# Kernel optimization log

Hardware: AMD Instinct MI355X
Metric: run time of the kernel (lower is better)

## Reference

```python
import jax, jax.numpy as jnp
import numpy as np

D = 768
HID = 4 * D
B = 16
HRES = 32
WRES = 32
T = HRES * WRES


def layernorm(x, g, b, eps=1e-5):
    m = jnp.mean(x, axis=-1, keepdims=True)
    v = jnp.mean(jnp.square(x - m), axis=-1, keepdims=True)
    return (x - m) * jax.lax.rsqrt(v + eps) * g + b


def q_shift(x, H, W):
    # Vision-RWKV quad-directional token shift: split channels into 4 groups,
    # each group takes the neighboring patch's value in one direction (zero pad).
    Bn, N, C = x.shape
    xi = x.reshape(Bn, H, W, C)
    c = C // 4
    g0 = jnp.pad(xi[:, :, :-1, 0 * c:1 * c], ((0, 0), (0, 0), (1, 0), (0, 0)))  # from left
    g1 = jnp.pad(xi[:, :, 1:, 1 * c:2 * c], ((0, 0), (0, 0), (0, 1), (0, 0)))   # from right
    g2 = jnp.pad(xi[:, :-1, :, 2 * c:3 * c], ((0, 0), (1, 0), (0, 0), (0, 0)))  # from above
    g3 = jnp.pad(xi[:, 1:, :, 3 * c:4 * c], ((0, 0), (0, 1), (0, 0), (0, 0)))   # from below
    return jnp.concatenate([g0, g1, g2, g3], axis=-1).reshape(Bn, N, C)


def wkv_scan(w_log, u, k, v):
    # Numerically stable RWKV WKV recurrence (per-channel linear attention).
    # k, v: [B, T, C]; w = -exp(w_log) is the per-channel decay, u the bonus.
    w = -jnp.exp(w_log)
    kT = jnp.swapaxes(k, 0, 1)  # [T, B, C]
    vT = jnp.swapaxes(v, 0, 1)
    Bn, C = k.shape[0], k.shape[2]
    aa0 = jnp.zeros((Bn, C), k.dtype)
    bb0 = jnp.zeros((Bn, C), k.dtype)
    pp0 = jnp.full((Bn, C), -1e30, k.dtype)

    def step(carry, kv):
        aa, bb, pp = carry
        kt, vt = kv
        ww = u + kt
        p = jnp.maximum(pp, ww)
        e1 = jnp.exp(pp - p)
        e2 = jnp.exp(ww - p)
        out = (e1 * aa + e2 * vt) / (e1 * bb + e2)
        ww2 = pp + w
        p2 = jnp.maximum(ww2, kt)
        e1b = jnp.exp(ww2 - p2)
        e2b = jnp.exp(kt - p2)
        return (e1b * aa + e2b * vt, e1b * bb + e2b, p2), out

    _, outT = jax.lax.scan(step, (aa0, bb0, pp0), (kT, vT))
    return jnp.swapaxes(outT, 0, 1)  # [B, T, C]


def setup_inputs() -> dict:
    key = jax.random.key(0)
    ks = jax.random.split(key, 16)

    def nrm(k, shape, s=0.02):
        return jax.random.normal(k, shape, jnp.float32) * s

    return {
        "x": jax.random.normal(ks[0], (B, T, D), jnp.float32),
        "H": HRES,
        "W": WRES,
        "ln1_g": jnp.ones((D,), jnp.float32),
        "ln1_b": jnp.zeros((D,), jnp.float32),
        "ln2_g": jnp.ones((D,), jnp.float32),
        "ln2_b": jnp.zeros((D,), jnp.float32),
        "mu_k": jax.random.uniform(ks[1], (D,), jnp.float32),
        "mu_v": jax.random.uniform(ks[2], (D,), jnp.float32),
        "mu_r": jax.random.uniform(ks[3], (D,), jnp.float32),
        "w_log": nrm(ks[4], (D,), 0.5),
        "u": nrm(ks[5], (D,), 0.5),
        "Wk": nrm(ks[6], (D, D)),
        "Wv": nrm(ks[7], (D, D)),
        "Wr": nrm(ks[8], (D, D)),
        "Wo": nrm(ks[9], (D, D)),
        "cmu_k": jax.random.uniform(ks[10], (D,), jnp.float32),
        "cmu_r": jax.random.uniform(ks[11], (D,), jnp.float32),
        "Ck": nrm(ks[12], (HID, D)),
        "Cv": nrm(ks[13], (D, HID)),
        "Cr": nrm(ks[14], (D, D)),
    }


def reference(x, H, W, ln1_g, ln1_b, ln2_g, ln2_b, mu_k, mu_v, mu_r, w_log, u,
              Wk, Wv, Wr, Wo, cmu_k, cmu_r, Ck, Cv, Cr):
    h = x
    # ---- spatial mix (RWKV time-mix over patch sequence) ----
    a = layernorm(h, ln1_g, ln1_b)
    sx = q_shift(a, H, W)
    xk = a * mu_k + sx * (1.0 - mu_k)
    xv = a * mu_v + sx * (1.0 - mu_v)
    xr = a * mu_r + sx * (1.0 - mu_r)
    k = xk @ Wk.T
    v = xv @ Wv.T
    r = jax.nn.sigmoid(xr @ Wr.T)
    wkv = wkv_scan(w_log, u, k, v)
    h = h + (r * wkv) @ Wo.T
    # ---- channel mix (squared-ReLU gated FFN) ----
    a2 = layernorm(h, ln2_g, ln2_b)
    sx2 = q_shift(a2, H, W)
    xk2 = a2 * cmu_k + sx2 * (1.0 - cmu_k)
    xr2 = a2 * cmu_r + sx2 * (1.0 - cmu_r)
    kk = jnp.square(jax.nn.relu(xk2 @ Ck.T))
    h = h + jax.nn.sigmoid(xr2 @ Cr.T) * (kk @ Cv.T)
    # ---- outer residual from RWKVBlock.forward ----
    return h + x
```

## Files before the change

### kernel.cpp

```cpp
#include <hip/hip_runtime.h>
#include <hip/hip_bf16.h>

#define DD   768
#define TT   1024
#define BBATCH 16
#define NROWS (BBATCH * TT)
#define HIDN 3072
#define HHALF 1536
#define HH 32
#define WW 32
#define DW  (DD * DD)
#define DH  (DD * HIDN)
#define CCH 64
#define PCH (TT / CCH)

typedef float  floatx4 __attribute__((ext_vector_type(4)));
typedef __bf16 bf16x8  __attribute__((ext_vector_type(8)));

__device__ __forceinline__ float bf2f(__hip_bfloat16 v) { return __bfloat162float(v); }
__device__ __forceinline__ __hip_bfloat16 f2bf(float v) { return __float2bfloat16(v); }
__device__ __forceinline__ float toF(__hip_bfloat16 v) { return __bfloat162float(v); }
__device__ __forceinline__ float toF(float v) { return v; }

__device__ __forceinline__ void load4f(const float* __restrict__ p, float o[4]) {
    const float4 v = *reinterpret_cast<const float4*>(p);
    o[0] = v.x; o[1] = v.y; o[2] = v.z; o[3] = v.w;
}
__device__ __forceinline__ void load4f(const __hip_bfloat16* __restrict__ p, float o[4]) {
    const ushort4 v = *reinterpret_cast<const ushort4*>(p);
    o[0] = bf2f(__hip_bfloat16_raw{v.x});
    o[1] = bf2f(__hip_bfloat16_raw{v.y});
    o[2] = bf2f(__hip_bfloat16_raw{v.z});
    o[3] = bf2f(__hip_bfloat16_raw{v.w});
}

#define GL2LDS(gp, lp)  __builtin_amdgcn_global_load_lds(                     \
    (const __attribute__((address_space(1))) void*)(gp),                      \
    (__attribute__((address_space(3))) void*)(lp), 16, 0, 0)

__global__ __launch_bounds__(256)
void cvt_all(const float* __restrict__ w0, const float* __restrict__ w1,
             const float* __restrict__ w2, const float* __restrict__ w3,
             const float* __restrict__ w4, const float* __restrict__ w5,
             const float* __restrict__ w6, __hip_bfloat16* __restrict__ dst)
{
    const int b = blockIdx.x;
    const float* s; size_t dofs; int rel;
    if (b < 2880) {
        const int seg = b / 576; rel = b - seg * 576;
        s = seg == 0 ? w0 : seg == 1 ? w1 : seg == 2 ? w2 : seg == 3 ? w3 : w4;
        dofs = (size_t)seg * DW;
    } else if (b < 5184) {
        rel = b - 2880; s = w5; dofs = 5ull * DW;
    } else {
        rel = b - 5184; s = w6; dofs = 5ull * DW + DH;
    }
    const int i = rel * 1024 + threadIdx.x * 4;
    const float4 v = *reinterpret_cast<const float4*>(s + i);
    __hip_bfloat16 o[4] = {f2bf(v.x), f2bf(v.y), f2bf(v.z), f2bf(v.w)};
    *reinterpret_cast<ushort4*>(&dst[dofs + i]) = *reinterpret_cast<const ushort4*>(o);
}

template <typename TIN>
__global__ __launch_bounds__(256)
void ln_stats_k(const TIN* __restrict__ x,
                float* __restrict__ mean, float* __restrict__ rstd)
{
    const int row  = blockIdx.x * 4 + (threadIdx.x >> 6);
    const int lane = threadIdx.x & 63;
    const TIN* xr = x + (size_t)row * DD;
    float s1 = 0.f, s2 = 0.f;
#pragma unroll
    for (int q = 0; q < 3; ++q) {
        float v4[4];
        load4f(xr + 4 * lane + 256 * q, v4);
#pragma unroll
        for (int e = 0; e < 4; ++e) { s1 += v4[e]; s2 += v4[e] * v4[e]; }
    }
#pragma unroll
    for (int off = 32; off > 0; off >>= 1) {
        s1 += __shfl_down(s1, off);
        s2 += __shfl_down(s2, off);
    }
    if (lane == 0) {
        const float m = s1 * (1.f / DD);
        mean[row] = m;
        rstd[row] = rsqrtf(s2 * (1.f / DD) - m * m + 1e-5f);
    }
}

template <typename TIN, int NOUT>
__global__ __launch_bounds__(256)
void mix_k(const TIN* __restrict__ x,
           const float* __restrict__ mean, const float* __restrict__ rstd,
           const float* __restrict__ g, const float* __restrict__ b,
           const float* __restrict__ muk,
           const float* __restrict__ muv,
           const float* __restrict__ mur,
           __hip_bfloat16* __restrict__ xk,
           __hip_bfloat16* __restrict__ xv,
           __hip_bfloat16* __restrict__ xr)
{
    const size_t i4 = ((size_t)blockIdx.x * 256 + threadIdx.x) * 4;
    const int c  = (int)(i4 % DD);
    const int n  = (int)((i4 / DD) % TT);
    const int bb = (int)(i4 / ((size_t)DD * TT));
    const int y = n >> 5, xp = n & 31;
    const int grow = bb * TT + n;

    const int grp = c / (DD / 4);
    int ny = y, nx = xp; bool ok;
    if      (grp == 0) { nx = xp - 1; ok = xp > 0;      }
    else if (grp == 1) { nx = xp + 1; ok = xp < WW - 1; }
    else if (grp == 2) { ny = y - 1;  ok = y > 0;       }
    else               { ny = y + 1;  ok = y < HH - 1;  }

    const float4 gv = *reinterpret_cast<const float4*>(g + c);
    const float4 bv = *reinterpret_cast<const float4*>(b + c);
    const float gg[4] = {gv.x, gv.y, gv.z, gv.w};
    const float bbv[4] = {bv.x, bv.y, bv.z, bv.w};

    float xc[4];
    load4f(x + (size_t)grow * DD + c, xc);
    const float m = mean[grow], rs = rstd[grow];
    float av[4], sx[4] = {0.f, 0.f, 0.f, 0.f};
#pragma unroll
    for (int e = 0; e < 4; ++e) av[e] = (xc[e] - m) * rs * gg[e] + bbv[e];

    if (ok) {
        const int nrow = bb * TT + ny * WW + nx;
        float xn[4];
        load4f(x + (size_t)nrow * DD + c, xn);
        const float m2 = mean[nrow], rs2 = rstd[nrow];
#pragma unroll
        for (int e = 0; e < 4; ++e) sx[e] = (xn[e] - m2) * rs2 * gg[e] + bbv[e];
    }

    const float4 mkv = *reinterpret_cast<const float4*>(muk + c);
    const float4 mrv = *reinterpret_cast<const float4*>(mur + c);
    const float mk[4] = {mkv.x, mkv.y, mkv.z, mkv.w};
    const float mr[4] = {mrv.x, mrv.y, mrv.z, mrv.w};
    __hip_bfloat16 ok4[4], or4[4];
#pragma unroll
    for (int e = 0; e < 4; ++e) {
        ok4[e] = f2bf(av[e] * mk[e] + sx[e] * (1.f - mk[e]));
        or4[e] = f2bf(av[e] * mr[e] + sx[e] * (1.f - mr[e]));
    }
    *reinterpret_cast<ushort4*>(&xk[i4]) = *reinterpret_cast<const ushort4*>(ok4);
    *reinterpret_cast<ushort4*>(&xr[i4]) = *reinterpret_cast<const ushort4*>(or4);
    if (NOUT == 3) {
        const float4 mvv = *reinterpret_cast<const float4*>(muv + c);
        const float mv[4] = {mvv.x, mvv.y, mvv.z, mvv.w};
        __hip_bfloat16 ov4[4];
#pragma unroll
        for (int e = 0; e < 4; ++e)
            ov4[e] = f2bf(av[e] * mv[e] + sx[e] * (1.f - mv[e]));
        *reinterpret_cast<ushort4*>(&xv[i4]) = *reinterpret_cast<const ushort4*>(ov4);
    }
}

#define BM 128
#define BN 128
#define BKK 64

__device__ __forceinline__ void gemm_core(
    const __hip_bfloat16* __restrict__ A, const __hip_bfloat16* __restrict__ W,
    int K, int Wstr, int bm, int bn, unsigned short* lds, floatx4 acc[4][4])
{
    const int tid  = threadIdx.x;
    const int lane = tid & 63, wid = tid >> 6;
    const int l15  = lane & 15, quad = lane >> 4;
    const int m0   = (wid & 1) * 64;
    const int n0   = (wid >> 1) * 64;
    const int srow  = lane >> 3;
    const int gcolg = (lane & 7) ^ srow;
    const int s0    = wid * 4;
    const int swzbase = l15 & 7;

    for (int k0 = 0; k0 < K; k0 += BKK) {
#pragma unroll
        for (int t = 0; t < 4; ++t) {
            const int s   = s0 + t;
            const int row = s * 8 + srow;
            GL2LDS(A + (size_t)(bm * BM + row) * K    + k0 + gcolg * 8,
                   &lds[s * 512]);
            GL2LDS(W + (size_t)(bn * BN + row) * Wstr + k0 + gcolg * 8,
                   &lds[8192 + s * 512]);
        }
        __syncthreads();
#pragma unroll
        for (int kk = 0; kk < BKK; kk += 32) {
            const int swz = (((kk >> 3) + quad) ^ swzbase) * 8;
            bf16x8 af[4], bfr[4];
#pragma unroll
            for (int i = 0; i < 4; ++i)
                af[i] = *reinterpret_cast<const bf16x8*>(
                    &lds[(m0 + i * 16 + l15) * BKK + swz]);
#pragma unroll
            for (int j = 0; j < 4; ++j)
                bfr[j] = *reinterpret_cast<const bf16x8*>(
                    &lds[8192 + (n0 + j * 16 + l15) * BKK + swz]);
#pragma unroll
            for (int i = 0; i < 4; ++i)
#pragma unroll
                for (int j = 0; j < 4; ++j)
                    acc[i][j] = __builtin_amdgcn_mfma_f32_16x16x32_bf16(
                        af[i], bfr[j], acc[i][j], 0, 0, 0);
        }
        __syncthreads();
    }
}

__device__ __forceinline__ void xpose_band(const floatx4 accRow[4], float* scr,
                                           int lane, float cv[16])
{
    const int l15 = lane & 15, quad = lane >> 4;
#pragma unroll
    for (int j = 0; j < 4; ++j)
#pragma unroll
        for (int r = 0; r < 4; ++r)
            scr[(quad * 4 + r) * 68 + j * 16 + l15] = accRow[j][r];
    const int row_l = lane >> 2, cb = (lane & 3) * 16;
#pragma unroll
    for (int q = 0; q < 4; ++q)
        *reinterpret_cast<float4*>(&cv[q * 4]) =
            *reinterpret_cast<const float4*>(&scr[row_l * 68 + cb + q * 4]);
}

template <int MODE>
__global__ __launch_bounds__(256, 2)
void gemm_bt(const __hip_bfloat16* __restrict__ A,
             const __hip_bfloat16* __restrict__ W,
             int K, int Wstr, int Nn,
             __hip_bfloat16* __restrict__ outB,
             float* __restrict__ outF,
             const __hip_bfloat16* __restrict__ auxS,
             const __hip_bfloat16* __restrict__ auxH,
             const float* __restrict__ auxX,
             const float* __restrict__ auxG)
{
    __shared__ __align__(16) unsigned short lds[16384];
    const int bm = blockIdx.x, bn = blockIdx.y;
    const int tid = threadIdx.x, lane = tid & 63, wid = tid >> 6;
    const int m0 = (wid & 1) * 64, n0 = (wid >> 1) * 64;

    floatx4 acc[4][4];
#pragma unroll
    for (int i = 0; i < 4; ++i)
#pragma unroll
        for (int j = 0; j < 4; ++j)
            acc[i][j] = floatx4{0.f, 0.f, 0.f, 0.f};

    gemm_core(A, W, K, Wstr, bm, bn, lds, acc);

    float* scr = reinterpret_cast<float*>(lds) + wid * 1088;
    const int row_l = lane >> 2, cb = (lane & 3) * 16;
#pragma unroll
    for (int i = 0; i < 4; ++i) {
        float cv[16];
        xpose_band(acc[i], scr, lane, cv);
        const int grow = bm * BM + m0 + i * 16 + row_l;
        const int gcol = bn * BN + n0 + cb;
        const size_t idx = (size_t)grow * Nn + gcol;
        if (MODE == 1 || MODE == 3) {
            __hip_bfloat16 ob[16];
#pragma unroll
            for (int e = 0; e < 16; ++e) {
                float v = cv[e];
                if (MODE == 1) v = 1.f / (1.f + __expf(-v));
                else { v = fmaxf(v, 0.f); v = v * v; }
                ob[e] = f2bf(v);
            }
            *reinterpret_cast<uint4*>(&outB[idx])     = *reinterpret_cast<const uint4*>(&ob[0]);
            *reinterpret_cast<uint4*>(&outB[idx + 8]) = *reinterpret_cast<const uint4*>(&ob[8]);
        } else if (MODE == 2) {
            float xv[16];
#pragma unroll
            for (int q = 0; q < 4; ++q)
                *reinterpret_cast<float4*>(&xv[q * 4]) =
                    *reinterpret_cast<const float4*>(&auxX[idx + q * 4]);
            __hip_bfloat16 ob[16];
#pragma unroll
            for (int e = 0; e < 16; ++e) ob[e] = f2bf(cv[e] + xv[e]);
            *reinterpret_cast<uint4*>(&outB[idx])     = *reinterpret_cast<const uint4*>(&ob[0]);
            *reinterpret_cast<uint4*>(&outB[idx + 8]) = *reinterpret_cast<const uint4*>(&ob[8]);
        } else if (MODE == 4) {
            unsigned short hs[16], ss[16]; float xv[16], ov[16];
            *reinterpret_cast<uint4*>(&hs[0]) = *reinterpret_cast<const uint4*>(&auxH[idx]);
            *reinterpret_cast<uint4*>(&hs[8]) = *reinterpret_cast<const uint4*>(&auxH[idx + 8]);
            *reinterpret_cast<uint4*>(&ss[0]) = *reinterpret_cast<const uint4*>(&auxS[idx]);
            *reinterpret_cast<uint4*>(&ss[8]) = *reinterpret_cast<const uint4*>(&auxS[idx + 8]);
#pragma unroll
            for (int q = 0; q < 4; ++q)
                *reinterpret_cast<float4*>(&xv[q * 4]) =
                    *reinterpret_cast<const float4*>(&auxX[idx + q * 4]);
#pragma unroll
            for (int e = 0; e < 16; ++e)
                ov[e] = bf2f(__hip_bfloat16_raw{hs[e]})
                      + bf2f(__hip_bfloat16_raw{ss[e]}) * cv[e] + xv[e];
#pragma unroll
            for (int q = 0; q < 4; ++q)
                *reinterpret_cast<float4*>(&outF[idx + q * 4]) =
                    *reinterpret_cast<const float4*>(&ov[q * 4]);
        } else if (MODE == 5) {
            unsigned short ss[16]; float ov[16];
            *reinterpret_cast<uint4*>(&ss[0]) = *reinterpret_cast<const uint4*>(&auxS[idx]);
            *reinterpret_cast<uint4*>(&ss[8]) = *reinterpret_cast<const uint4*>(&auxS[idx + 8]);
#pragma unroll
            for (int q = 0; q < 4; ++q)
                *reinterpret_cast<float4*>(&ov[q * 4]) =
                    *reinterpret_cast<const float4*>(&outF[idx + q * 4]);
#pragma unroll
            for (int e = 0; e < 16; ++e)
                ov[e] += bf2f(__hip_bfloat16_raw{ss[e]}) * cv[e];
#pragma unroll
            for (int q = 0; q < 4; ++q)
                *reinterpret_cast<float4*>(&outF[idx + q * 4]) =
                    *reinterpret_cast<const float4*>(&ov[q * 4]);
        } else if (MODE == 6) {
            unsigned short hs[16]; float xv[16], gf[16], ov[16];
            *reinterpret_cast<uint4*>(&hs[0]) = *reinterpret_cast<const uint4*>(&auxH[idx]);
            *reinterpret_cast<uint4*>(&hs[8]) = *reinterpret_cast<const uint4*>(&auxH[idx + 8]);
#pragma unroll
            for (int q = 0; q < 4; ++q) {
                *reinterpret_cast<float4*>(&xv[q * 4]) =
                    *reinterpret_cast<const float4*>(&auxX[idx + q * 4]);
                *reinterpret_cast<float4*>(&gf[q * 4]) =
                    *reinterpret_cast<const float4*>(&auxG[idx + q * 4]);
            }
#pragma unroll
            for (int e = 0; e < 16; ++e)
                ov[e] = bf2f(__hip_bfloat16_raw{hs[e]}) + gf[e] * cv[e] + xv[e];
#pragma unroll
            for (int q = 0; q < 4; ++q)
                *reinterpret_cast<float4*>(&outF[idx + q * 4]) =
                    *reinterpret_cast<const float4*>(&ov[q * 4]);
        } else {
            float ov[16];
#pragma unroll
            for (int e = 0; e < 16; ++e)
                ov[e] = 1.f / (1.f + __expf(-cv[e]));
#pragma unroll
            for (int q = 0; q < 4; ++q)
                *reinterpret_cast<float4*>(&outF[idx + q * 4]) =
                    *reinterpret_cast<const float4*>(&ov[q * 4]);
        }
    }
}

__global__ __launch_bounds__(256, 2)
void gemm_qkv(const __hip_bfloat16* __restrict__ A0, const __hip_bfloat16* __restrict__ A1,
              const __hip_bfloat16* __restrict__ A2,
              const __hip_bfloat16* __restrict__ W0, const __hip_bfloat16* __restrict__ W1,
              const __hip_bfloat16* __restrict__ W2,
              __hip_bfloat16* __restrict__ O0, __hip_bfloat16* __restrict__ O1,
              __hip_bfloat16* __restrict__ O2)
{
    __shared__ __align__(16) unsigned short lds[16384];
    const int z = blockIdx.z;
    const __hip_bfloat16* A = z == 0 ? A0 : z == 1 ? A1 : A2;
    const __hip_bfloat16* W = z == 0 ? W0 : z == 1 ? W1 : W2;
    __hip_bfloat16*       O = z == 0 ? O0 : z == 1 ? O1 : O2;
    const int bm = blockIdx.x, bn = blockIdx.y;
    const int tid = threadIdx.x, lane = tid & 63, wid = tid >> 6;
    const int m0 = (wid & 1) * 64, n0 = (wid >> 1) * 64;

    floatx4 acc[4][4];
#pragma unroll
    for (int i = 0; i < 4; ++i)
#pragma unroll
        for (int j = 0; j < 4; ++j)
            acc[i][j] = floatx4{0.f, 0.f, 0.f, 0.f};

    gemm_core(A, W, DD, DD, bm, bn, lds, acc);

    float* scr = reinterpret_cast<float*>(lds) + wid * 1088;
    const int row_l = lane >> 2, cb = (lane & 3) * 16;
#pragma unroll
    for (int i = 0; i < 4; ++i) {
        float cv[16];
        xpose_band(acc[i], scr, lane, cv);
        const int grow = bm * BM + m0 + i * 16 + row_l;
        const int gcol = bn * BN + n0 + cb;
        const size_t idx = (size_t)grow * DD + gcol;
        __hip_bfloat16 ob[16];
#pragma unroll
        for (int e = 0; e < 16; ++e) {
            float v = cv[e];
            if (z == 2) v = 1.f / (1.f + __expf(-v));
            ob[e] = f2bf(v);
        }
        *reinterpret_cast<uint4*>(&O[idx])     = *reinterpret_cast<const uint4*>(&ob[0]);
        *reinterpret_cast<uint4*>(&O[idx + 8]) = *reinterpret_cast<const uint4*>(&ob[8]);
    }
}

__global__ __launch_bounds__(256)
void wkv_passA(const float* __restrict__ w_log,
               const __hip_bfloat16* __restrict__ k,
               const __hip_bfloat16* __restrict__ v,
               float* __restrict__ SA, float* __restrict__ SB,
               float* __restrict__ SP)
{
    const int c  = blockIdx.x * 256 + threadIdx.x;
    const int j  = blockIdx.y;
    const int bb = blockIdx.z;
    const float w = -__expf(w_log[c]);
    const size_t base = ((size_t)bb * TT + j * CCH) * DD + c;
    float a = 0.f, b = 0.f, p = -1e30f;
#pragma unroll 4
    for (int t = 0; t < CCH; ++t) {
        const size_t o = base + (size_t)t * DD;
        const float kt = bf2f(k[o]);
        const float vt = bf2f(v[o]);
        const float ww2 = p + w;
        const float p2  = fmaxf(ww2, kt);
        const float e1  = __expf(ww2 - p2);
        const float e2  = __expf(kt - p2);
        a = e1 * a + e2 * vt;
        b = e1 * b + e2;
        p = p2;
    }
    const size_t si = ((size_t)bb * PCH + j) * DD + c;
    SA[si] = a; SB[si] = b; SP[si] = p;
}

__global__ __launch_bounds__(256)
void wkv_scanj(const float* __restrict__ w_log,
               float* __restrict__ SA, float* __restrict__ SB,
               float* __restrict__ SP)
{
    const int idx = blockIdx.x * 256 + threadIdx.x;
    const int c = idx % DD, bb = idx / DD;
    const float wC = -__expf(w_log[c]) * (float)CCH;
    float a = 0.f, b = 0.f, p = -1e30f;
#pragma unroll
    for (int j = 0; j < PCH; ++j) {
        const size_t si = ((size_t)bb * PCH + j) * DD + c;
        const float aj = SA[si], bj = SB[si], pj = SP[si];
        SA[si] = a; SB[si] = b; SP[si] = p;
        const float pd = p + wC;
        const float pn = fmaxf(pd, pj);
        const float e1 = __expf(pd - pn);
        const float e2 = __expf(pj - pn);
        a = e1 * a + e2 * aj;
        b = e1 * b + e2 * bj;
        p = pn;
    }
}

__global__ __launch_bounds__(256)
void wkv_passB(const float* __restrict__ w_log, const float* __restrict__ u,
               const __hip_bfloat16* __restrict__ k,
               const __hip_bfloat16* __restrict__ v,
               const __hip_bfloat16* __restrict__ r,
               __hip_bfloat16* __restrict__ rw,
               const float* __restrict__ SA, const float* __restrict__ SB,
               const float* __restrict__ SP)
{
    const int c  = blockIdx.x * 256 + threadIdx.x;
    const int j  = blockIdx.y;
    const int bb = blockIdx.z;
    const float w  = -__expf(w_log[c]);
    const float uu = u[c];
    const size_t si = ((size_t)bb * PCH + j) * DD + c;
    float aa = SA[si], bbv = SB[si], pp = SP[si];
    const size_t base = ((size_t)bb * TT + j * CCH) * DD + c;
#pragma unroll 4
    for (int t = 0; t < CCH; ++t) {
        const size_t o = base + (size_t)t * DD;
        const float kt = bf2f(k[o]);
        const float vt = bf2f(v[o]);
        const float rt = bf2f(r[o]);
        const float ww = uu + kt;
        const float p  = fmaxf(pp, ww);
        const float e1 = __expf(pp - p);
        const float e2 = __expf(ww - p);
        const float ov = __fdividef(e1 * aa + e2 * vt, e1 * bbv + e2);
        rw[o] = f2bf(rt * ov);
        const float ww2 = pp + w;
        const float p2  = fmaxf(ww2, kt);
        const float e1b = __expf(ww2 - p2);
        const float e2b = __expf(kt - p2);
        aa  = e1b * aa + e2b * vt;
        bbv = e1b * bbv + e2b;
        pp  = p2;
    }
}

extern "C" void kernel_launch(void* const* d_in, const int* in_sizes, int n_in,
                              void* d_out, int out_size, void* d_ws, size_t ws_size,
                              hipStream_t stream)
{
    (void)in_sizes; (void)n_in; (void)out_size;
    const float* x     = (const float*)d_in[0];
    const float* ln1_g = (const float*)d_in[3];
    const float* ln1_b = (const float*)d_in[4];
    const float* ln2_g = (const float*)d_in[5];
    const float* ln2_b = (const float*)d_in[6];
    const float* mu_k  = (const float*)d_in[7];
    const float* mu_v  = (const float*)d_in[8];
    const float* mu_r  = (const float*)d_in[9];
    const float* w_log = (const float*)d_in[10];
    const float* u     = (const float*)d_in[11];
    const float* Wk    = (const float*)d_in[12];
    const float* Wv    = (const float*)d_in[13];
    const float* Wr    = (const float*)d_in[14];
    const float* Wo    = (const float*)d_in[15];
    const float* cmu_k = (const float*)d_in[16];
    const float* cmu_r = (const float*)d_in[17];
    const float* Ck    = (const float*)d_in[18];
    const float* Cv    = (const float*)d_in[19];
    const float* Cr    = (const float*)d_in[20];
    float* out = (float*)d_out;

    const size_t ND = (size_t)NROWS * DD;
    const size_t SL = ND * 2;
    const size_t WBYTES = (size_t)(5 * DW + 2 * DH) * 2;
    const size_t NSTATE = (size_t)BBATCH * PCH * DD;
    const size_t TAIL = WBYTES + 2 * (size_t)NROWS * sizeof(float)
                      + 3 * NSTATE * sizeof(float);
    int nslots;
    if      (ws_size >= 7 * SL + TAIL) nslots = 7;
    else if (ws_size >= 6 * SL + TAIL) nslots = 6;
    else if (ws_size >= 5 * SL + TAIL) nslots = 5;
    else return;

    char* w = (char*)d_ws;
    __hip_bfloat16* S0 = (__hip_bfloat16*)(w);
    __hip_bfloat16* S1 = (__hip_bfloat16*)(w + 1 * SL);
    __hip_bfloat16* S2 = (__hip_bfloat16*)(w + 2 * SL);
    __hip_bfloat16* S3 = (__hip_bfloat16*)(w + 3 * SL);
    __hip_bfloat16* S4 = (__hip_bfloat16*)(w + 4 * SL);
    __hip_bfloat16* S5 = (__hip_bfloat16*)(w + 5 * SL);
    __hip_bfloat16* WB  = (__hip_bfloat16*)(w + (size_t)nslots * SL);
    __hip_bfloat16* WkB = WB;
    __hip_bfloat16* WvB = WB + 1ull * DW;
    __hip_bfloat16* WrB = WB + 2ull * DW;
    __hip_bfloat16* WoB = WB + 3ull * DW;
    __hip_bfloat16* CrB = WB + 4ull * DW;
    __hip_bfloat16* CkB = WB + 5ull * DW;
    __hip_bfloat16* CvB = CkB + DH;
    float* meanB = (float*)(w + (size_t)nslots * SL + WBYTES);
    float* rstdB = meanB + NROWS;
    float* SAb = rstdB + NROWS;
    float* SBb = SAb + NSTATE;
    float* SPb = SBb + NSTATE;

    const int LN_GRID  = NROWS / 4;
    const int MIX_GRID = (int)(ND / 1024);
    const dim3 g768(NROWS / BM, DD / BN);
    const dim3 g1536(NROWS / BM, HHALF / BN);
    const dim3 gCk(NROWS / BM, HIDN / BN);
    const dim3 gqkv3(NROWS / BM, DD / BN, 3);
    const dim3 gqkv2(NROWS / BM, DD / BN, 2);
    const dim3 gwkv(DD / 256, PCH, BBATCH);

    cvt_all<<<7488, 256, 0, stream>>>(Wk, Wv, Wr, Wo, Cr, Ck, Cv, WB);

    ln_stats_k<float><<<LN_GRID, 256, 0, stream>>>(x, meanB, rstdB);
    mix_k<float, 3><<<MIX_GRID, 256, 0, stream>>>(x, meanB, rstdB, ln1_g, ln1_b,
                                                  mu_k, mu_v, mu_r, S0, S1, S2);

    if (nslots == 7) {
        gemm_qkv<<<gqkv3, 256, 0, stream>>>(S0, S1, S2, WkB, WvB, WrB, S3, S4, S5);
        wkv_passA<<<gwkv, 256, 0, stream>>>(w_log, S3, S4, SAb, SBb, SPb);
        wkv_scanj<<<(BBATCH * DD) / 256, 256, 0, stream>>>(w_log, SAb, SBb, SPb);
        wkv_passB<<<gwkv, 256, 0, stream>>>(w_log, u, S3, S4, S5, S1, SAb, SBb, SPb);
        gemm_bt<2><<<g768, 256, 0, stream>>>(S1, WoB, DD, DD, DD, S2, nullptr,
                                             nullptr, nullptr, x, nullptr);
        ln_stats_k<__hip_bfloat16><<<LN_GRID, 256, 0, stream>>>(S2, meanB, rstdB);
        mix_k<__hip_bfloat16, 2><<<MIX_GRID, 256, 0, stream>>>(S2, meanB, rstdB, ln2_g, ln2_b,
                                                               cmu_k, nullptr, cmu_r,
                                                               S0, nullptr, S3);
        gemm_bt<1><<<g768, 256, 0, stream>>>(S3, CrB, DD, DD, DD, S1, nullptr,
                                             nullptr, nullptr, nullptr, nullptr);
        gemm_bt<3><<<gCk, 256, 0, stream>>>(S0, CkB, DD, DD, HIDN,
                                            S3, nullptr, nullptr, nullptr, nullptr, nullptr);
        gemm_bt<4><<<g768, 256, 0, stream>>>(S3, CvB, HIDN, HIDN, DD,
                                             nullptr, out, S1, S2, x, nullptr);
    } else if (nslots == 6) {
        gemm_qkv<<<gqkv3, 256, 0, stream>>>(S0, S1, S2, WkB, WvB, WrB, S3, S4, S5);
        wkv_passA<<<gwkv, 256, 0, stream>>>(w_log, S3, S4, SAb, SBb, SPb);
        wkv_scanj<<<(BBATCH * DD) / 256, 256, 0, stream>>>(w_log, SAb, SBb, SPb);
        wkv_passB<<<gwkv, 256, 0, stream>>>(w_log, u, S3, S4, S5, S0, SAb, SBb, SPb);
        gemm_bt<2><<<g768, 256, 0, stream>>>(S0, WoB, DD, DD, DD, S1, nullptr,
                                             nullptr, nullptr, x, nullptr);
        ln_stats_k<__hip_bfloat16><<<LN_GRID, 256, 0, stream>>>(S1, meanB, rstdB);
        mix_k<__hip_bfloat16, 2><<<MIX_GRID, 256, 0, stream>>>(S1, meanB, rstdB, ln2_g, ln2_b,
                                                               cmu_k, nullptr, cmu_r,
                                                               S0, nullptr, S2);
        gemm_bt<7><<<g768, 256, 0, stream>>>(S2, CrB, DD, DD, DD, nullptr, out,
                                             nullptr, nullptr, nullptr, nullptr);
        gemm_bt<3><<<gCk, 256, 0, stream>>>(S0, CkB, DD, DD, HIDN,
                                            S2, nullptr, nullptr, nullptr, nullptr, nullptr);
        gemm_bt<6><<<g768, 256, 0, stream>>>(S2, CvB, HIDN, HIDN, DD,
                                             nullptr, out, nullptr, S1, x, out);
    } else {
        gemm_qkv<<<gqkv2, 256, 0, stream>>>(S0, S1, nullptr, WkB, WvB, nullptr,
                                            S3, S4, nullptr);
        gemm_bt<1><<<g768, 256, 0, stream>>>(S2, WrB, DD, DD, DD, S0, nullptr,
                                             nullptr, nullptr, nullptr, nullptr);
        wkv_passA<<<gwkv, 256, 0, stream>>>(w_log, S3, S4, SAb, SBb, SPb);
        wkv_scanj<<<(BBATCH * DD) / 256, 256, 0, stream>>>(w_log, SAb, SBb, SPb);
        wkv_passB<<<gwkv, 256, 0, stream>>>(w_log, u, S3, S4, S0, S1, SAb, SBb, SPb);
        gemm_bt<2><<<g768, 256, 0, stream>>>(S1, WoB, DD, DD, DD, S2, nullptr,
                                             nullptr, nullptr, x, nullptr);
        ln_stats_k<__hip_bfloat16><<<LN_GRID, 256, 0, stream>>>(S2, meanB, rstdB);
        mix_k<__hip_bfloat16, 2><<<MIX_GRID, 256, 0, stream>>>(S2, meanB, rstdB, ln2_g, ln2_b,
                                                               cmu_k, nullptr, cmu_r,
                                                               S0, nullptr, S3);
        gemm_bt<1><<<g768, 256, 0, stream>>>(S3, CrB, DD, DD, DD, S1, nullptr,
                                             nullptr, nullptr, nullptr, nullptr);
        __hip_bfloat16* kk = S3;
        gemm_bt<3><<<g1536, 256, 0, stream>>>(S0, CkB, DD, DD, HHALF,
                                              kk, nullptr, nullptr, nullptr, nullptr, nullptr);
        gemm_bt<4><<<g768, 256, 0, stream>>>(kk, CvB, HHALF, HIDN, DD,
                                             nullptr, out, S1, S2, x, nullptr);
        gemm_bt<3><<<g1536, 256, 0, stream>>>(S0, CkB + (size_t)HHALF * DD, DD, DD, HHALF,
                                              kk, nullptr, nullptr, nullptr, nullptr, nullptr);
        gemm_bt<5><<<g768, 256, 0, stream>>>(kk, CvB + HHALF, HHALF, HIDN, DD,
                                             nullptr, out, S1, nullptr, nullptr, nullptr);
    }
}
```

Baseline: 534.4 us.

## Replace 128x128 GEMMs with 256x256-tile pipelined 512-thread GEMM kernel

Adds a new GEMM kernel that computes 256x256 output tiles with 8 waves and 128KB of LDS. It double-buffers global-to-LDS loads, interleaving staged prefetch of the next k-tiles with MFMA quarters, and uses explicit barriers, vmcnt waits and setprio. Blocks are remapped with an XCD-aware swizzle. The 7- and 6-slot paths switch all projection and FFN GEMMs to this kernel to raise data reuse and overlap memory with compute. The risks are lower occupancy, fewer blocks per GEMM (192 for the 768-wide outputs), and fragile hand-written waitcnt logic.

```diff
diff --git a/kernel.cpp b/kernel.cpp
--- a/kernel.cpp
+++ b/kernel.cpp
@@ -38,6 +38,13 @@
     (const __attribute__((address_space(1))) void*)(gp),                      \
     (__attribute__((address_space(3))) void*)(lp), 16, 0, 0)
 
+#define BARX() do { asm volatile("" ::: "memory");                             \
+    __builtin_amdgcn_s_barrier();                                              \
+    asm volatile("" ::: "memory");                                             \
+    __builtin_amdgcn_sched_barrier(0); } while (0)
+#define WAITV6() asm volatile("s_waitcnt vmcnt(6)" ::: "memory")
+#define WAITV0() asm volatile("s_waitcnt vmcnt(0)" ::: "memory")
+
 __global__ __launch_bounds__(256)
 void cvt_all(const float* __restrict__ w0, const float* __restrict__ w1,
              const float* __restrict__ w2, const float* __restrict__ w3,
@@ -159,6 +166,293 @@
     }
 }
 
+__device__ __forceinline__ void xpose_band(const floatx4 accRow[4], float* scr,
+                                           int lane, float cv[16])
+{
+    const int l15 = lane & 15, quad = lane >> 4;
+#pragma unroll
+    for (int j = 0; j < 4; ++j)
+#pragma unroll
+        for (int r = 0; r < 4; ++r)
+            scr[(quad * 4 + r) * 68 + j * 16 + l15] = accRow[j][r];
+    const int row_l = lane >> 2, cb = (lane & 3) * 16;
+#pragma unroll
+    for (int q = 0; q < 4; ++q)
+        *reinterpret_cast<float4*>(&cv[q * 4]) =
+            *reinterpret_cast<const float4*>(&scr[row_l * 68 + cb + q * 4]);
+}
+
+template <int MODE>
+__device__ __forceinline__ void mode_store(
+    const float cv[16], size_t idx,
+    __hip_bfloat16* __restrict__ outB, float* __restrict__ outF,
+    const __hip_bfloat16* __restrict__ auxS, const __hip_bfloat16* __restrict__ auxH,
+    const float* __restrict__ auxX, const float* __restrict__ auxG)
+{
+    if (MODE == 1 || MODE == 3) {
+        __hip_bfloat16 ob[16];
+#pragma unroll
+        for (int e = 0; e < 16; ++e) {
+            float v = cv[e];
+            if (MODE == 1) v = 1.f / (1.f + __expf(-v));
+            else { v = fmaxf(v, 0.f); v = v * v; }
+            ob[e] = f2bf(v);
+        }
+        *reinterpret_cast<uint4*>(&outB[idx])     = *reinterpret_cast<const uint4*>(&ob[0]);
+        *reinterpret_cast<uint4*>(&outB[idx + 8]) = *reinterpret_cast<const uint4*>(&ob[8]);
+    } else if (MODE == 2) {
+        float xv[16];
+#pragma unroll
+        for (int q = 0; q < 4; ++q)
+            *reinterpret_cast<float4*>(&xv[q * 4]) =
+                *reinterpret_cast<const float4*>(&auxX[idx + q * 4]);
+        __hip_bfloat16 ob[16];
+#pragma unroll
+        for (int e = 0; e < 16; ++e) ob[e] = f2bf(cv[e] + xv[e]);
+        *reinterpret_cast<uint4*>(&outB[idx])     = *reinterpret_cast<const uint4*>(&ob[0]);
+        *reinterpret_cast<uint4*>(&outB[idx + 8]) = *reinterpret_cast<const uint4*>(&ob[8]);
+    } else if (MODE == 4) {
+        unsigned short hs[16], ss[16]; float xv[16], ov[16];
+        *reinterpret_cast<uint4*>(&hs[0]) = *reinterpret_cast<const uint4*>(&auxH[idx]);
+        *reinterpret_cast<uint4*>(&hs[8]) = *reinterpret_cast<const uint4*>(&auxH[idx + 8]);
+        *reinterpret_cast<uint4*>(&ss[0]) = *reinterpret_cast<const uint4*>(&auxS[idx]);
+        *reinterpret_cast<uint4*>(&ss[8]) = *reinterpret_cast<const uint4*>(&auxS[idx + 8]);
+#pragma unroll
+        for (int q = 0; q < 4; ++q)
+            *reinterpret_cast<float4*>(&xv[q * 4]) =
+                *reinterpret_cast<const float4*>(&auxX[idx + q * 4]);
+#pragma unroll
+        for (int e = 0; e < 16; ++e)
+            ov[e] = bf2f(__hip_bfloat16_raw{hs[e]})
+                  + bf2f(__hip_bfloat16_raw{ss[e]}) * cv[e] + xv[e];
+#pragma unroll
+        for (int q = 0; q < 4; ++q)
+            *reinterpret_cast<float4*>(&outF[idx + q * 4]) =
+                *reinterpret_cast<const float4*>(&ov[q * 4]);
+    } else if (MODE == 5) {
+        unsigned short ss[16]; float ov[16];
+        *reinterpret_cast<uint4*>(&ss[0]) = *reinterpret_cast<const uint4*>(&auxS[idx]);
+        *reinterpret_cast<uint4*>(&ss[8]) = *reinterpret_cast<const uint4*>(&auxS[idx + 8]);
+#pragma unroll
+        for (int q = 0; q < 4; ++q)
+            *reinterpret_cast<float4*>(&ov[q * 4]) =
+                *reinterpret_cast<const float4*>(&outF[idx + q * 4]);
+#pragma unroll
+        for (int e = 0; e < 16; ++e)
+            ov[e] += bf2f(__hip_bfloat16_raw{ss[e]}) * cv[e];
+#pragma unroll
+        for (int q = 0; q < 4; ++q)
+            *reinterpret_cast<float4*>(&outF[idx + q * 4]) =
+                *reinterpret_cast<const float4*>(&ov[q * 4]);
+    } else if (MODE == 6) {
+        unsigned short hs[16]; float xv[16], gf[16], ov[16];
+        *reinterpret_cast<uint4*>(&hs[0]) = *reinterpret_cast<const uint4*>(&auxH[idx]);
+        *reinterpret_cast<uint4*>(&hs[8]) = *reinterpret_cast<const uint4*>(&auxH[idx + 8]);
+#pragma unroll
+        for (int q = 0; q < 4; ++q) {
+            *reinterpret_cast<float4*>(&xv[q * 4]) =
+                *reinterpret_cast<const float4*>(&auxX[idx + q * 4]);
+            *reinterpret_cast<float4*>(&gf[q * 4]) =
+                *reinterpret_cast<const float4*>(&auxG[idx + q * 4]);
+        }
+#pragma unroll
+        for (int e = 0; e < 16; ++e)
+            ov[e] = bf2f(__hip_bfloat16_raw{hs[e]}) + gf[e] * cv[e] + xv[e];
+#pragma unroll
+        for (int q = 0; q < 4; ++q)
+            *reinterpret_cast<float4*>(&outF[idx + q * 4]) =
+                *reinterpret_cast<const float4*>(&ov[q * 4]);
+    } else {
+        float ov[16];
+#pragma unroll
+        for (int e = 0; e < 16; ++e)
+            ov[e] = 1.f / (1.f + __expf(-cv[e]));
+#pragma unroll
+        for (int q = 0; q < 4; ++q)
+            *reinterpret_cast<float4*>(&outF[idx + q * 4]) =
+                *reinterpret_cast<const float4*>(&ov[q * 4]);
+    }
+}
+
+#define STG256(tau, j)                                                         \
+  do { if ((tau) * 64 < K) {                                                   \
+    const int _sb = ((((tau) & 1) * 4) + (j)) * 8192;                          \
+    const int _k0 = (tau) * 64;                                                \
+    const __hip_bfloat16 *_s0, *_s1;                                           \
+    if ((j) < 2) {                                                             \
+      _s0 = A + (size_t)(bmr + (j) * 128 + r0) * K + _k0 + colg;               \
+      _s1 = A + (size_t)(bmr + (j) * 128 + r1) * K + _k0 + colg;               \
+    } else {                                                                   \
+      const int _w0 = bnr + ((j) == 2 ? 128 : 0);                              \
+      _s0 = W + (size_t)(_w0 + r0) * Wstr + _k0 + colg;                        \
+      _s1 = W + (size_t)(_w0 + r1) * Wstr + _k0 + colg;                        \
+    }                                                                          \
+    GL2LDS(_s0, &lds[_sb + wid * 512]);                                        \
+    GL2LDS(_s1, &lds[_sb + 4096 + wid * 512]);                                 \
+  } } while (0)
+
+#define LDA_ALL(buf)                                                           \
+  { const int _ab = ((buf) * 4 + wr) * 8192;                                   \
+    _Pragma("unroll") for (int mf = 0; mf < 8; ++mf)                           \
+    _Pragma("unroll") for (int k2 = 0; k2 < 2; ++k2)                           \
+      af[mf][k2] = *reinterpret_cast<const bf16x8*>(                           \
+        &lds[_ab + (mf * 16 + l15) * 64 + (((k2 * 4 + quad) ^ sw7) * 8)]); }
+
+#define LDB_NH(buf, nh)                                                        \
+  { const int _bb = ((buf) * 4 + ((wc >> 1) ? 2 : 3)) * 8192;                  \
+    _Pragma("unroll") for (int nf = 0; nf < 2; ++nf)                           \
+    _Pragma("unroll") for (int k2 = 0; k2 < 2; ++k2)                           \
+      bfx[nf][k2] = *reinterpret_cast<const bf16x8*>(                          \
+        &lds[_bb + ((wc & 1) * 64 + (nh) * 32 + nf * 16 + l15) * 64            \
+             + (((k2 * 4 + quad) ^ sw7) * 8)]); }
+
+#define MFQ(MH, NH)                                                            \
+  _Pragma("unroll") for (int mf = 0; mf < 4; ++mf)                             \
+  _Pragma("unroll") for (int nf = 0; nf < 2; ++nf)                             \
+  _Pragma("unroll") for (int k2 = 0; k2 < 2; ++k2)                             \
+    acc[(MH) * 4 + mf][(NH) * 2 + nf] =                                        \
+      __builtin_amdgcn_mfma_f32_16x16x32_bf16(af[(MH) * 4 + mf][k2],           \
+        bfx[nf][k2], acc[(MH) * 4 + mf][(NH) * 2 + nf], 0, 0, 0);
+
+#define TILE_STEP(tt, buf)                                                     \
+  {                                                                            \
+    LDA_ALL(buf); LDB_NH(buf, 0);                                              \
+    STG256((tt) + 1, 3);                                                       \
+    BARX();                                                                    \
+    __builtin_amdgcn_s_setprio(1); MFQ(0, 0); __builtin_amdgcn_s_setprio(0);   \
+    BARX();                                                                    \
+    STG256((tt) + 2, 0);                                                       \
+    BARX();                                                                    \
+    __builtin_amdgcn_s_setprio(1); MFQ(1, 0); __builtin_amdgcn_s_setprio(0);   \
+    BARX();                                                                    \
+    LDB_NH(buf, 1);                                                            \
+    STG256((tt) + 2, 1);                                                       \
+    BARX();                                                                    \
+    __builtin_amdgcn_s_setprio(1); MFQ(0, 1); __builtin_amdgcn_s_setprio(0);   \
+    BARX();                                                                    \
+    STG256((tt) + 2, 2);                                                       \
+    BARX();                                                                    \
+    __builtin_amdgcn_s_setprio(1); MFQ(1, 1); __builtin_amdgcn_s_setprio(0);   \
+    if ((tt) + 2 == nt) { WAITV0(); } else { WAITV6(); }                       \
+    BARX();                                                                    \
+  }
+
+struct G256Ctx {
+    int bm, bn;
+    int tid, lane, wid, wr, wc, l15, quad, sw7, r0, r1, colg;
+};
+
+__device__ __forceinline__ void g256_decode(G256Ctx& c, int b, int nbn, int nwg)
+{
+    const int s = (b & 7) * (nwg >> 3) + (b >> 3);
+    c.bm = s / nbn; c.bn = s % nbn;
+    c.tid = threadIdx.x; c.lane = c.tid & 63; c.wid = c.tid >> 6;
+    c.wr = c.wid >> 2; c.wc = c.wid & 3;
+    c.l15 = c.lane & 15; c.quad = c.lane >> 4; c.sw7 = c.l15 & 7;
+    c.r0 = c.tid >> 3; c.r1 = c.r0 + 64;
+    c.colg = ((c.tid & 7) ^ (c.r0 & 7)) * 8;
+}
+
+__device__ __forceinline__ void g256_core(
+    const __hip_bfloat16* __restrict__ A, const __hip_bfloat16* __restrict__ W,
+    int K, int Wstr, const G256Ctx& c, unsigned short* lds, floatx4 acc[8][4])
+{
+    const int bmr = c.bm * 256, bnr = c.bn * 256;
+    const int wid = c.wid, wr = c.wr, wc = c.wc;
+    const int l15 = c.l15, quad = c.quad, sw7 = c.sw7;
+    const int r0 = c.r0, r1 = c.r1, colg = c.colg;
+    const int nt = K >> 6;
+
+    bf16x8 af[8][2], bfx[2][2];
+
+    STG256(0, 0); STG256(0, 1); STG256(0, 2); STG256(0, 3);
+    STG256(1, 0); STG256(1, 1); STG256(1, 2);
+    WAITV6();
+    BARX();
+
+    for (int t = 0; t < nt; t += 2) {
+        TILE_STEP(t, 0);
+        TILE_STEP(t + 1, 1);
+    }
+    WAITV0();
+}
+
+template <int MODE>
+__global__ __launch_bounds__(512, 2)
+void gemm256(const __hip_bfloat16* __restrict__ A, const __hip_bfloat16* __restrict__ W,
+             int K, int Wstr, int Nn,
+             __hip_bfloat16* __restrict__ outB, float* __restrict__ outF,
+             const __hip_bfloat16* __restrict__ auxS, const __hip_bfloat16* __restrict__ auxH,
+             const float* __restrict__ auxX, const float* __restrict__ auxG)
+{
+    __shared__ __align__(16) unsigned short lds[65536];
+    G256Ctx c; g256_decode(c, blockIdx.x, Nn >> 8, gridDim.x);
+
+    floatx4 acc[8][4];
+#pragma unroll
+    for (int i = 0; i < 8; ++i)
+#pragma unroll
+        for (int j = 0; j < 4; ++j) acc[i][j] = floatx4{0.f, 0.f, 0.f, 0.f};
+
+    g256_core(A, W, K, Wstr, c, lds, acc);
+
+    float* scr = reinterpret_cast<float*>(lds) + c.wid * 1088;
+    const int row_l = c.lane >> 2, cb = (c.lane & 3) * 16;
+#pragma unroll
+    for (int i = 0; i < 8; ++i) {
+        float cv[16];
+        xpose_band(acc[i], scr, c.lane, cv);
+        const int grow = c.bm * 256 + c.wr * 128 + i * 16 + row_l;
+        const int gcol = c.bn * 256 + c.wc * 64 + cb;
+        const size_t idx = (size_t)grow * Nn + gcol;
+        mode_store<MODE>(cv, idx, outB, outF, auxS, auxH, auxX, auxG);
+    }
+}
+
+__global__ __launch_bounds__(512, 2)
+void gemm256_qkv(const __hip_bfloat16* __restrict__ A0, const __hip_bfloat16* __restrict__ A1,
+                 const __hip_bfloat16* __restrict__ A2,
+                 const __hip_bfloat16* __restrict__ W0, const __hip_bfloat16* __restrict__ W1,
+                 const __hip_bfloat16* __restrict__ W2,
+                 __hip_bfloat16* __restrict__ O0, __hip_bfloat16* __restrict__ O1,
+                 __hip_bfloat16* __restrict__ O2)
+{
+    __shared__ __align__(16) unsigned short lds[65536];
+    const int z = blockIdx.z;
+    const __hip_bfloat16* A = z == 0 ? A0 : z == 1 ? A1 : A2;
+    const __hip_bfloat16* W = z == 0 ? W0 : z == 1 ? W1 : W2;
+    __hip_bfloat16*       O = z == 0 ? O0 : z == 1 ? O1 : O2;
+    G256Ctx c; g256_decode(c, blockIdx.x, DD >> 8, gridDim.x);
+
+    floatx4 acc[8][4];
+#pragma unroll
+    for (int i = 0; i < 8; ++i)
+#pragma unroll
+        for (int j = 0; j < 4; ++j) acc[i][j] = floatx4{0.f, 0.f, 0.f, 0.f};
+
+    g256_core(A, W, DD, DD, c, lds, acc);
+
+    float* scr = reinterpret_cast<float*>(lds) + c.wid * 1088;
+    const int row_l = c.lane >> 2, cb = (c.lane & 3) * 16;
+#pragma unroll
+    for (int i = 0; i < 8; ++i) {
+        float cv[16];
+        xpose_band(acc[i], scr, c.lane, cv);
+        const int grow = c.bm * 256 + c.wr * 128 + i * 16 + row_l;
+        const int gcol = c.bn * 256 + c.wc * 64 + cb;
+        const size_t idx = (size_t)grow * DD + gcol;
+        __hip_bfloat16 ob[16];
+#pragma unroll
+        for (int e = 0; e < 16; ++e) {
+            float v = cv[e];
+            if (z == 2) v = 1.f / (1.f + __expf(-v));
+            ob[e] = f2bf(v);
+        }
+        *reinterpret_cast<uint4*>(&O[idx])     = *reinterpret_cast<const uint4*>(&ob[0]);
+        *reinterpret_cast<uint4*>(&O[idx + 8]) = *reinterpret_cast<const uint4*>(&ob[8]);
+    }
+}
+
 #define BM 128
 #define BN 128
 #define BKK 64
@@ -191,10 +485,10 @@
 #pragma unroll
         for (int kk = 0; kk < BKK; kk += 32) {
             const int swz = (((kk >> 3) + quad) ^ swzbase) * 8;
-            bf16x8 af[4], bfr[4];
+            bf16x8 afr[4], bfr[4];
 #pragma unroll
             for (int i = 0; i < 4; ++i)
-                af[i] = *reinterpret_cast<const bf16x8*>(
+                afr[i] = *reinterpret_cast<const bf16x8*>(
                     &lds[(m0 + i * 16 + l15) * BKK + swz]);
 #pragma unroll
             for (int j = 0; j < 4; ++j)
@@ -205,26 +499,10 @@
 #pragma unroll
                 for (int j = 0; j < 4; ++j)
                     acc[i][j] = __builtin_amdgcn_mfma_f32_16x16x32_bf16(
-                        af[i], bfr[j], acc[i][j], 0, 0, 0);
+                        afr[i], bfr[j], acc[i][j], 0, 0, 0);
         }
         __syncthreads();
     }
-}
-
-__device__ __forceinline__ void xpose_band(const floatx4 accRow[4], float* scr,
-                                           int lane, float cv[16])
-{
-    const int l15 = lane & 15, quad = lane >> 4;
-#pragma unroll
-    for (int j = 0; j < 4; ++j)
-#pragma unroll
-        for (int r = 0; r < 4; ++r)
-            scr[(quad * 4 + r) * 68 + j * 16 + l15] = accRow[j][r];
-    const int row_l = lane >> 2, cb = (lane & 3) * 16;
-#pragma unroll
-    for (int q = 0; q < 4; ++q)
-        *reinterpret_cast<float4*>(&cv[q * 4]) =
-            *reinterpret_cast<const float4*>(&scr[row_l * 68 + cb + q * 4]);
 }
 
 template <int MODE>
@@ -262,89 +540,7 @@
         const int grow = bm * BM + m0 + i * 16 + row_l;
         const int gcol = bn * BN + n0 + cb;
         const size_t idx = (size_t)grow * Nn + gcol;
-        if (MODE == 1 || MODE == 3) {
-            __hip_bfloat16 ob[16];
-#pragma unroll
-            for (int e = 0; e < 16; ++e) {
-                float v = cv[e];
-                if (MODE == 1) v = 1.f / (1.f + __expf(-v));
-                else { v = fmaxf(v, 0.f); v = v * v; }
-                ob[e] = f2bf(v);
-            }
-            *reinterpret_cast<uint4*>(&outB[idx])     = *reinterpret_cast<const uint4*>(&ob[0]);
-            *reinterpret_cast<uint4*>(&outB[idx + 8]) = *reinterpret_cast<const uint4*>(&ob[8]);
-        } else if (MODE == 2) {
-            float xv[16];
-#pragma unroll
-            for (int q = 0; q < 4; ++q)
-                *reinterpret_cast<float4*>(&xv[q * 4]) =
-                    *reinterpret_cast<const float4*>(&auxX[idx + q * 4]);
-            __hip_bfloat16 ob[16];
-#pragma unroll
-            for (int e = 0; e < 16; ++e) ob[e] = f2bf(cv[e] + xv[e]);
-            *reinterpret_cast<uint4*>(&outB[idx])     = *reinterpret_cast<const uint4*>(&ob[0]);
-            *reinterpret_cast<uint4*>(&outB[idx + 8]) = *reinterpret_cast<const uint4*>(&ob[8]);
-        } else if (MODE == 4) {
-            unsigned short hs[16], ss[16]; float xv[16], ov[16];
-            *reinterpret_cast<uint4*>(&hs[0]) = *reinterpret_cast<const uint4*>(&auxH[idx]);
-            *reinterpret_cast<uint4*>(&hs[8]) = *reinterpret_cast<const uint4*>(&auxH[idx + 8]);
-            *reinterpret_cast<uint4*>(&ss[0]) = *reinterpret_cast<const uint4*>(&auxS[idx]);
-            *reinterpret_cast<uint4*>(&ss[8]) = *reinterpret_cast<const uint4*>(&auxS[idx + 8]);
-#pragma unroll
-            for (int q = 0; q < 4; ++q)
-                *reinterpret_cast<float4*>(&xv[q * 4]) =
-                    *reinterpret_cast<const float4*>(&auxX[idx + q * 4]);
-#pragma unroll
-            for (int e = 0; e < 16; ++e)
-                ov[e] = bf2f(__hip_bfloat16_raw{hs[e]})
-                      + bf2f(__hip_bfloat16_raw{ss[e]}) * cv[e] + xv[e];
-#pragma unroll
-            for (int q = 0; q < 4; ++q)
-                *reinterpret_cast<float4*>(&outF[idx + q * 4]) =
-                    *reinterpret_cast<const float4*>(&ov[q * 4]);
-        } else if (MODE == 5) {
-            unsigned short ss[16]; float ov[16];
-            *reinterpret_cast<uint4*>(&ss[0]) = *reinterpret_cast<const uint4*>(&auxS[idx]);
-            *reinterpret_cast<uint4*>(&ss[8]) = *reinterpret_cast<const uint4*>(&auxS[idx + 8]);
-#pragma unroll
-            for (int q = 0; q < 4; ++q)
-                *reinterpret_cast<float4*>(&ov[q * 4]) =
-                    *reinterpret_cast<const float4*>(&outF[idx + q * 4]);
-#pragma unroll
-            for (int e = 0; e < 16; ++e)
-                ov[e] += bf2f(__hip_bfloat16_raw{ss[e]}) * cv[e];
-#pragma unroll
-            for (int q = 0; q < 4; ++q)
-                *reinterpret_cast<float4*>(&outF[idx + q * 4]) =
-                    *reinterpret_cast<const float4*>(&ov[q * 4]);
-        } else if (MODE == 6) {
-            unsigned short hs[16]; float xv[16], gf[16], ov[16];
-            *reinterpret_cast<uint4*>(&hs[0]) = *reinterpret_cast<const uint4*>(&auxH[idx]);
-            *reinterpret_cast<uint4*>(&hs[8]) = *reinterpret_cast<const uint4*>(&auxH[idx + 8]);
-#pragma unroll
-            for (int q = 0; q < 4; ++q) {
-                *reinterpret_cast<float4*>(&xv[q * 4]) =
-                    *reinterpret_cast<const float4*>(&auxX[idx + q * 4]);
-                *reinterpret_cast<float4*>(&gf[q * 4]) =
-                    *reinterpret_cast<const float4*>(&auxG[idx + q * 4]);
-            }
-#pragma unroll
-            for (int e = 0; e < 16; ++e)
-                ov[e] = bf2f(__hip_bfloat16_raw{hs[e]}) + gf[e] * cv[e] + xv[e];
-#pragma unroll
-            for (int q = 0; q < 4; ++q)
-                *reinterpret_cast<float4*>(&outF[idx + q * 4]) =
-                    *reinterpret_cast<const float4*>(&ov[q * 4]);
-        } else {
-            float ov[16];
-#pragma unroll
-            for (int e = 0; e < 16; ++e)
-                ov[e] = 1.f / (1.f + __expf(-cv[e]));
-#pragma unroll
-            for (int q = 0; q < 4; ++q)
-                *reinterpret_cast<float4*>(&outF[idx + q * 4]) =
-                    *reinterpret_cast<const float4*>(&ov[q * 4]);
-        }
+        mode_store<MODE>(cv, idx, outB, outF, auxS, auxH, auxX, auxG);
     }
 }
 
@@ -549,12 +745,10 @@
 
     const int LN_GRID  = NROWS / 4;
     const int MIX_GRID = (int)(ND / 1024);
-    const dim3 g768(NROWS / BM, DD / BN);
-    const dim3 g1536(NROWS / BM, HHALF / BN);
-    const dim3 gCk(NROWS / BM, HIDN / BN);
-    const dim3 gqkv3(NROWS / BM, DD / BN, 3);
-    const dim3 gqkv2(NROWS / BM, DD / BN, 2);
     const dim3 gwkv(DD / 256, PCH, BBATCH);
+    const int G768  = (NROWS / 256) * (DD / 256);
+    const int GHID  = (NROWS / 256) * (HIDN / 256);
+    const dim3 gq256(G768, 1, 3);
 
     cvt_all<<<7488, 256, 0, stream>>>(Wk, Wv, Wr, Wo, Cr, Ck, Cv, WB);
 
@@ -563,42 +757,44 @@
                                                   mu_k, mu_v, mu_r, S0, S1, S2);
 
     if (nslots == 7) {
-        gemm_qkv<<<gqkv3, 256, 0, stream>>>(S0, S1, S2, WkB, WvB, WrB, S3, S4, S5);
+        gemm256_qkv<<<gq256, 512, 0, stream>>>(S0, S1, S2, WkB, WvB, WrB, S3, S4, S5);
         wkv_passA<<<gwkv, 256, 0, stream>>>(w_log, S3, S4, SAb, SBb, SPb);
         wkv_scanj<<<(BBATCH * DD) / 256, 256, 0, stream>>>(w_log, SAb, SBb, SPb);
         wkv_passB<<<gwkv, 256, 0, stream>>>(w_log, u, S3, S4, S5, S1, SAb, SBb, SPb);
-        gemm_bt<2><<<g768, 256, 0, stream>>>(S1, WoB, DD, DD, DD, S2, nullptr,
+        gemm256<2><<<G768, 512, 0, stream>>>(S1, WoB, DD, DD, DD, S2, nullptr,
                                              nullptr, nullptr, x, nullptr);
         ln_stats_k<__hip_bfloat16><<<LN_GRID, 256, 0, stream>>>(S2, meanB, rstdB);
         mix_k<__hip_bfloat16, 2><<<MIX_GRID, 256, 0, stream>>>(S2, meanB, rstdB, ln2_g, ln2_b,
                                                                cmu_k, nullptr, cmu_r,
                                                                S0, nullptr, S3);
-        gemm_bt<1><<<g768, 256, 0, stream>>>(S3, CrB, DD, DD, DD, S1, nullptr,
+        gemm256<1><<<G768, 512, 0, stream>>>(S3, CrB, DD, DD, DD, S1, nullptr,
                                              nullptr, nullptr, nullptr, nullptr);
-        gemm_bt<3><<<gCk, 256, 0, stream>>>(S0, CkB, DD, DD, HIDN,
-                                            S3, nullptr, nullptr, nullptr, nullptr, nullptr);
-        gemm_bt<4><<<g768, 256, 0, stream>>>(S3, CvB, HIDN, HIDN, DD,
+        gemm256<3><<<GHID, 512, 0, stream>>>(S0, CkB, DD, DD, HIDN,
+                                             S3, nullptr, nullptr, nullptr, nullptr, nullptr);
+        gemm256<4><<<G768, 512, 0, stream>>>(S3, CvB, HIDN, HIDN, DD,
                                              nullptr, out, S1, S2, x, nullptr);
     } else if (nslots == 6) {
-        gemm_qkv<<<gqkv3, 256, 0, stream>>>(S0, S1, S2, WkB, WvB, WrB, S3, S4, S5);
+        gemm256_qkv<<<gq256, 512, 0, stream>>>(S0, S1, S2, WkB, WvB, WrB, S3, S4, S5);
         wkv_passA<<<gwkv, 256, 0, stream>>>(w_log, S3, S4, SAb, SBb, SPb);
         wkv_scanj<<<(BBATCH * DD) / 256, 256, 0, stream>>>(w_log, SAb, SBb, SPb);
         wkv_passB<<<gwkv, 256, 0, stream>>>(w_log, u, S3, S4, S5, S0, SAb, SBb, SPb);
-        gemm_bt<2><<<g768, 256, 0, stream>>>(S0, WoB, DD, DD, DD, S1, nullptr,
+        gemm256<2><<<G768, 512, 0, stream>>>(S0, WoB, DD, DD, DD, S1, nullptr,
                                              nullptr, nullptr, x, nullptr);
         ln_stats_k<__hip_bfloat16><<<LN_GRID, 256, 0, stream>>>(S1, meanB, rstdB);
         mix_k<__hip_bfloat16, 2><<<MIX_GRID, 256, 0, stream>>>(S1, meanB, rstdB, ln2_g, ln2_b,
                                                                cmu_k, nullptr, cmu_r,
                                                                S0, nullptr, S2);
-        gemm_bt<7><<<g768, 256, 0, stream>>>(S2, CrB, DD, DD, DD, nullptr, out,
+        gemm256<7><<<G768, 512, 0, stream>>>(S2, CrB, DD, DD, DD, nullptr, out,
                                              nullptr, nullptr, nullptr, nullptr);
-        gemm_bt<3><<<gCk, 256, 0, stream>>>(S0, CkB, DD, DD, HIDN,
-                                            S2, nullptr, nullptr, nullptr, nullptr, nullptr);
-        gemm_bt<6><<<g768, 256, 0, stream>>>(S2, CvB, HIDN, HIDN, DD,
+        gemm256<3><<<GHID, 512, 0, stream>>>(S0, CkB, DD, DD, HIDN,
+                                             S2, nullptr, nullptr, nullptr, nullptr, nullptr);
+        gemm256<6><<<G768, 512, 0, stream>>>(S2, CvB, HIDN, HIDN, DD,
                                              nullptr, out, nullptr, S1, x, out);
     } else {
-        gemm_qkv<<<gqkv2, 256, 0, stream>>>(S0, S1, nullptr, WkB, WvB, nullptr,
-                                            S3, S4, nullptr);
+        const dim3 g768(NROWS / BM, DD / BN);
+        const dim3 g1536(NROWS / BM, HHALF / BN);
+        gemm_qkv<<<dim3(NROWS / BM, DD / BN, 2), 256, 0, stream>>>(
+            S0, S1, nullptr, WkB, WvB, nullptr, S3, S4, nullptr);
         gemm_bt<1><<<g768, 256, 0, stream>>>(S2, WrB, DD, DD, DD, S0, nullptr,
                                              nullptr, nullptr, nullptr, nullptr);
         wkv_passA<<<gwkv, 256, 0, stream>>>(w_log, S3, S4, SAb, SBb, SPb);
```

Result: slower. 661.9 us (+23.9%).
